# Optimization experiments

Hardware: AMD Instinct MI355X
Metric: run time of the kernel (lower is better)

Reference implementation:

```python
import jax, jax.numpy as jnp
import numpy as np

def setup_inputs() -> dict:
    key = jax.random.key(0)
    ks = jax.random.split(key, 6)
    B, H, Dk, Dv = 128, 16, 128, 128
    return {
        "q": jax.random.normal(ks[0], (B, H, 1, Dk), dtype=jnp.float32),
        "k": jax.random.normal(ks[1], (B, H, 1, Dk), dtype=jnp.float32),
        "v": jax.random.normal(ks[2], (B, H, 1, Dv), dtype=jnp.float32),
        "g": jax.random.uniform(ks[3], (B, H, 1), dtype=jnp.float32),
        "beta": jax.random.uniform(ks[4], (B, H, 1), dtype=jnp.float32),
        "last_recurrent_state": jax.random.normal(ks[5], (B, H, Dk, Dv), dtype=jnp.float32),
    }

def reference(q, k, v, g, beta, last_recurrent_state):
    # q,k: (B,H,1,Dk); v: (B,H,1,Dv); g,beta: (B,H,1); state: (B,H,Dk,Dv)
    q_t = q[:, :, 0, :]                      # (B,H,Dk)
    k_t = k[:, :, 0, :]                      # (B,H,Dk)
    v_t = v[:, :, 0, :]                      # (B,H,Dv)
    decay = jnp.exp(g)[..., None]            # (B,H,1,1)
    state = last_recurrent_state * decay     # (B,H,Dk,Dv)
    kv_mem = jnp.einsum('bhkv,bhk->bhv', state, k_t)   # (B,H,Dv)
    delta = (v_t - kv_mem) * beta            # (B,H,Dv)
    state = state + k_t[..., :, None] * delta[..., None, :]  # outer update
    out = jnp.einsum('bhkv,bhk->bhv', state, q_t)       # (B,H,Dv)
    out = out[:, :, None, :]                 # (B,H,1,Dv)
    return jnp.concatenate([out.reshape(-1), state.reshape(-1)], axis=0)
```

## Files before the change

### kernel.cpp

```cpp
#include <hip/hip_runtime.h>
#include <hip/hip_bf16.h>


#define DK 128
#define DV 128

__global__ __launch_bounds__(256) void s1_cell_kernel(
    const float* __restrict__ q,
    const float* __restrict__ k,
    const float* __restrict__ v,
    const float* __restrict__ g,
    const float* __restrict__ beta,
    const float* __restrict__ S,
    float* __restrict__ out,
    int BH)
{
    const int bh = blockIdx.x;
    const size_t stile = (size_t)bh * DK * DV;
    const float* __restrict__ Sb   = S + stile;
    float* __restrict__ out_o      = out + (size_t)bh * DV;
    float* __restrict__ out_S      = out + (size_t)BH * DV + stile;

    __shared__ float kt[DK];
    __shared__ float qt[DK];
    __shared__ float vt[DV];
    __shared__ float apart[8][DV];
    __shared__ float bpart[8][DV];
    __shared__ float sdelta[DV];
    __shared__ float s_kq;

    const int t = threadIdx.x;

    if (t < DK) {
        kt[t] = k[bh * DK + t];
        qt[t] = q[bh * DK + t];
        vt[t] = v[bh * DV + t];
    }
    __syncthreads();

    const float decay = expf(g[bh]);
    const float bta   = beta[bh];

    if (t < 64) {
        float val = kt[t] * qt[t] + kt[t + 64] * qt[t + 64];
        #pragma unroll
        for (int off = 32; off > 0; off >>= 1)
            val += __shfl_down(val, off, 64);
        if (t == 0) s_kq = val;
    }

    const int vb = (t & 31) * 4;
    const int kb = (t >> 5) * 16;

    float4 s[16];
    float a0 = 0.f, a1 = 0.f, a2 = 0.f, a3 = 0.f;
    float b0 = 0.f, b1 = 0.f, b2 = 0.f, b3 = 0.f;

    #pragma unroll
    for (int i = 0; i < 16; ++i) {
        const int kk = kb + i;
        s[i] = *(const float4*)(Sb + (size_t)kk * DV + vb);
        const float kv = kt[kk];
        const float qv = qt[kk];
        a0 += s[i].x * kv;  a1 += s[i].y * kv;  a2 += s[i].z * kv;  a3 += s[i].w * kv;
        b0 += s[i].x * qv;  b1 += s[i].y * qv;  b2 += s[i].z * qv;  b3 += s[i].w * qv;
    }
    const int grp = t >> 5;
    apart[grp][vb + 0] = a0;  apart[grp][vb + 1] = a1;
    apart[grp][vb + 2] = a2;  apart[grp][vb + 3] = a3;
    bpart[grp][vb + 0] = b0;  bpart[grp][vb + 1] = b1;
    bpart[grp][vb + 2] = b2;  bpart[grp][vb + 3] = b3;
    __syncthreads();

    if (t < DV) {
        float A = 0.f, Bq = 0.f;
        #pragma unroll
        for (int j = 0; j < 8; ++j) {
            A  += apart[j][t];
            Bq += bpart[j][t];
        }
        const float dlt = (vt[t] - decay * A) * bta;
        sdelta[t] = dlt;
        out_o[t] = decay * Bq + s_kq * dlt;
    }
    __syncthreads();

    const float d0 = sdelta[vb + 0];
    const float d1 = sdelta[vb + 1];
    const float d2 = sdelta[vb + 2];
    const float d3 = sdelta[vb + 3];

    #pragma unroll
    for (int i = 0; i < 16; ++i) {
        const int kk = kb + i;
        const float ktk = kt[kk];
        float4 r;
        r.x = decay * s[i].x + ktk * d0;
        r.y = decay * s[i].y + ktk * d1;
        r.z = decay * s[i].z + ktk * d2;
        r.w = decay * s[i].w + ktk * d3;
        *(float4*)(out_S + (size_t)kk * DV + vb) = r;
    }
}

extern "C" void kernel_launch(void* const* d_in, const int* in_sizes, int n_in,
                              void* d_out, int out_size, void* d_ws, size_t ws_size,
                              hipStream_t stream) {
    const float* q    = (const float*)d_in[0];
    const float* k    = (const float*)d_in[1];
    const float* v    = (const float*)d_in[2];
    const float* g    = (const float*)d_in[3];
    const float* beta = (const float*)d_in[4];
    const float* S    = (const float*)d_in[5];
    float* out = (float*)d_out;

    const int BH = in_sizes[3];

    s1_cell_kernel<<<BH, 256, 0, stream>>>(q, k, v, g, beta, S, out, BH);
}
```

Baseline: 244.8 us.

## Split each head's state across four blocks by value columns, use nontemporal stores

Each (b,h) state tile is now handled by four blocks, each owning 32 value columns. Every thread holds 4 rows instead of 16, which cuts register pressure and raises the block count for better occupancy and latency hiding on this memory-bound update. Output and state writes use nontemporal stores to avoid polluting cache. In exchange, k and q are reloaded four times, the shared-memory partial reduction grows to 32 steps, and each row segment read is only 128 bytes wide.

```diff
diff --git a/kernel.cpp b/kernel.cpp
--- a/kernel.cpp
+++ b/kernel.cpp
@@ -1,9 +1,10 @@
 #include <hip/hip_runtime.h>
-#include <hip/hip_bf16.h>
 
 
 #define DK 128
 #define DV 128
+#define VS 32
+typedef float f4 __attribute__((ext_vector_type(4)));
 
 __global__ __launch_bounds__(256) void s1_cell_kernel(
     const float* __restrict__ q,
@@ -15,18 +16,21 @@
     float* __restrict__ out,
     int BH)
 {
-    const int bh = blockIdx.x;
+    const int bh    = blockIdx.x >> 2;
+    const int sl    = blockIdx.x & 3;
+    const int vbase = sl * VS;
+
     const size_t stile = (size_t)bh * DK * DV;
-    const float* __restrict__ Sb   = S + stile;
-    float* __restrict__ out_o      = out + (size_t)bh * DV;
-    float* __restrict__ out_S      = out + (size_t)BH * DV + stile;
+    const float* __restrict__ Sb   = S + stile + vbase;
+    float* __restrict__ out_o      = out + (size_t)bh * DV + vbase;
+    float* __restrict__ out_S      = out + (size_t)BH * DV + stile + vbase;
 
     __shared__ float kt[DK];
     __shared__ float qt[DK];
-    __shared__ float vt[DV];
-    __shared__ float apart[8][DV];
-    __shared__ float bpart[8][DV];
-    __shared__ float sdelta[DV];
+    __shared__ float vt[VS];
+    __shared__ float apart[32][VS];
+    __shared__ float bpart[32][VS];
+    __shared__ float sdelta[VS];
     __shared__ float s_kq;
 
     const int t = threadIdx.x;
@@ -34,8 +38,8 @@
     if (t < DK) {
         kt[t] = k[bh * DK + t];
         qt[t] = q[bh * DK + t];
-        vt[t] = v[bh * DV + t];
     }
+    if (t < VS) vt[t] = v[bh * DV + vbase + t];
     __syncthreads();
 
     const float decay = expf(g[bh]);
@@ -49,57 +53,51 @@
         if (t == 0) s_kq = val;
     }
 
-    const int vb = (t & 31) * 4;
-    const int kb = (t >> 5) * 16;
+    const int vc = (t & 7) * 4;
+    const int rb = t >> 3;
 
-    float4 s[16];
+    f4 s[4];
     float a0 = 0.f, a1 = 0.f, a2 = 0.f, a3 = 0.f;
     float b0 = 0.f, b1 = 0.f, b2 = 0.f, b3 = 0.f;
 
     #pragma unroll
-    for (int i = 0; i < 16; ++i) {
-        const int kk = kb + i;
-        s[i] = *(const float4*)(Sb + (size_t)kk * DV + vb);
-        const float kv = kt[kk];
-        const float qv = qt[kk];
+    for (int i = 0; i < 4; ++i) {
+        const int r = rb + 32 * i;
+        s[i] = *(const f4*)(Sb + (size_t)r * DV + vc);
+        const float kv = kt[r];
+        const float qv = qt[r];
         a0 += s[i].x * kv;  a1 += s[i].y * kv;  a2 += s[i].z * kv;  a3 += s[i].w * kv;
         b0 += s[i].x * qv;  b1 += s[i].y * qv;  b2 += s[i].z * qv;  b3 += s[i].w * qv;
     }
-    const int grp = t >> 5;
-    apart[grp][vb + 0] = a0;  apart[grp][vb + 1] = a1;
-    apart[grp][vb + 2] = a2;  apart[grp][vb + 3] = a3;
-    bpart[grp][vb + 0] = b0;  bpart[grp][vb + 1] = b1;
-    bpart[grp][vb + 2] = b2;  bpart[grp][vb + 3] = b3;
+    *(f4*)&apart[rb][vc] = (f4){a0, a1, a2, a3};
+    *(f4*)&bpart[rb][vc] = (f4){b0, b1, b2, b3};
     __syncthreads();
 
-    if (t < DV) {
+    if (t < VS) {
         float A = 0.f, Bq = 0.f;
         #pragma unroll
-        for (int j = 0; j < 8; ++j) {
+        for (int j = 0; j < 32; ++j) {
             A  += apart[j][t];
             Bq += bpart[j][t];
         }
         const float dlt = (vt[t] - decay * A) * bta;
         sdelta[t] = dlt;
-        out_o[t] = decay * Bq + s_kq * dlt;
+        __builtin_nontemporal_store(decay * Bq + s_kq * dlt, &out_o[t]);
     }
     __syncthreads();
 
-    const float d0 = sdelta[vb + 0];
-    const float d1 = sdelta[vb + 1];
-    const float d2 = sdelta[vb + 2];
-    const float d3 = sdelta[vb + 3];
+    const f4 d = *(const f4*)&sdelta[vc];
 
     #pragma unroll
-    for (int i = 0; i < 16; ++i) {
-        const int kk = kb + i;
-        const float ktk = kt[kk];
-        float4 r;
-        r.x = decay * s[i].x + ktk * d0;
-        r.y = decay * s[i].y + ktk * d1;
-        r.z = decay * s[i].z + ktk * d2;
-        r.w = decay * s[i].w + ktk * d3;
-        *(float4*)(out_S + (size_t)kk * DV + vb) = r;
+    for (int i = 0; i < 4; ++i) {
+        const int r = rb + 32 * i;
+        const float ktk = kt[r];
+        f4 w;
+        w.x = decay * s[i].x + ktk * d.x;
+        w.y = decay * s[i].y + ktk * d.y;
+        w.z = decay * s[i].z + ktk * d.z;
+        w.w = decay * s[i].w + ktk * d.w;
+        __builtin_nontemporal_store(w, (f4*)(out_S + (size_t)r * DV + vc));
     }
 }
 
@@ -116,5 +114,5 @@
 
     const int BH = in_sizes[3];
 
-    s1_cell_kernel<<<BH, 256, 0, stream>>>(q, k, v, g, beta, S, out, BH);
+    s1_cell_kernel<<<BH * 4, 256, 0, stream>>>(q, k, v, g, beta, S, out, BH);
 }
```

Measured after the change: 248.7 us. No clear change (+1.6%).
